# Kernel optimization log

Hardware: AMD Instinct MI355X
Metric: run time of the kernel (lower is better)

Reference implementation:

```python
import jax, jax.numpy as jnp
import numpy as np
from jax import lax

BN_EPS = 1e-5
SQ_EPS = 1e-8


def squash(s, axis=-1):
    # v = (|s|^2 / (1+|s|^2)) * s / |s|
    n2 = jnp.sum(s * s, axis=axis, keepdims=True)
    return (n2 / (1.0 + n2)) * s / jnp.sqrt(n2 + SQ_EPS)


def setup_inputs() -> dict:
    key = jax.random.key(0)
    ks = jax.random.split(key, 5)
    B, C, H, W = 64, 512, 28, 28
    NUM_ROUTES = 8 * 10 * 10  # lower_num_caps * 10 * 10 after k9 s2 conv on 28x28
    features = jax.random.normal(ks[0], (B, C, H, W), jnp.float32)
    conv1_w = jax.random.normal(ks[1], (256, 512, 3, 3), jnp.float32) * 0.02
    conv1_b = jnp.zeros((256,), jnp.float32)
    bn_gamma = jnp.ones((256,), jnp.float32)
    bn_beta = jnp.zeros((256,), jnp.float32)
    bn_mean = jnp.zeros((256,), jnp.float32)
    bn_var = jnp.ones((256,), jnp.float32)
    prim_w = jax.random.normal(ks[2], (256, 256, 9, 9), jnp.float32) * 0.02
    prim_b = jnp.zeros((256,), jnp.float32)
    # routing transform: (num_routes, higher_num_caps, out_dim, in_dim)
    route_w = jax.random.normal(ks[3], (NUM_ROUTES, 2, 16, 32), jnp.float32) * 0.05
    return {"features": features, "conv1_w": conv1_w, "conv1_b": conv1_b,
            "bn_gamma": bn_gamma, "bn_beta": bn_beta, "bn_mean": bn_mean,
            "bn_var": bn_var, "prim_w": prim_w, "prim_b": prim_b,
            "route_w": route_w}


def reference(features, conv1_w, conv1_b, bn_gamma, bn_beta, bn_mean, bn_var,
              prim_w, prim_b, route_w):
    B = features.shape[0]
    dn = ("NCHW", "OIHW", "NCHW")
    # pre_conv: Conv2d(512->256, k3, pad1) + BatchNorm (eval) + ReLU
    x = lax.conv_general_dilated(features, conv1_w, (1, 1), "SAME",
                                 dimension_numbers=dn)
    x = x + conv1_b[None, :, None, None]
    inv = bn_gamma * lax.rsqrt(bn_var + BN_EPS)
    x = x * inv[None, :, None, None] + (bn_beta - bn_mean * inv)[None, :, None, None]
    x = jax.nn.relu(x)
    # primary capsules: Conv2d(256->8*32, k9, s2, valid) -> (B,256,10,10)
    p = lax.conv_general_dilated(x, prim_w, (2, 2), "VALID",
                                 dimension_numbers=dn)
    p = p + prim_b[None, :, None, None]
    Hp, Wp = p.shape[2], p.shape[3]
    # (B, num_caps, cap_dim, Hp*Wp) -> (B, num_caps*Hp*Wp, cap_dim)
    p = p.reshape(B, 8, 32, Hp * Wp).transpose(0, 1, 3, 2).reshape(B, 8 * Hp * Wp, 32)
    lower_caps = squash(p, axis=-1)  # (B, 800, 32)
    # predictions u_hat: (B, routes, higher_caps, out_dim)
    u_hat = jnp.einsum("bri,rjoi->brjo", lower_caps, route_w)
    # dynamic routing-by-agreement
    b = jnp.zeros((B, u_hat.shape[1], u_hat.shape[2]), u_hat.dtype)
    n_iter = 3
    for it in range(n_iter):
        c = jax.nn.softmax(b, axis=2)                  # coupling coeffs
        s = jnp.einsum("brj,brjo->bjo", c, u_hat)      # weighted sum
        v = squash(s, axis=-1)                          # (B, 2, 16)
        if it < n_iter - 1:
            b = b + jnp.einsum("brjo,bjo->brj", u_hat, v)
    return (lower_caps, v)
```

## Files before the change

### kernel.cpp

```cpp
#include <hip/hip_runtime.h>
#include <hip/hip_bf16.h>

#define BN_EPS 1e-5f
#define SQ_EPS 1e-8f

typedef __hip_bfloat16 bf16;
typedef __attribute__((ext_vector_type(8))) short bf16x8;
typedef __attribute__((ext_vector_type(4))) float f32x4;

__device__ __forceinline__ void gload_lds16(const void* g, void* l) {
    __builtin_amdgcn_global_load_lds(
        (const __attribute__((address_space(1))) unsigned int*)g,
        (__attribute__((address_space(3))) unsigned int*)l, 16, 0, 0);
}

__device__ __forceinline__ unsigned short f2bfu(float f) {
    bf16 h = __float2bfloat16(f);
    return *(unsigned short*)&h;
}

__global__ __launch_bounds__(256) void feat_to_nhwc(
    const float* __restrict__ feat, bf16* __restrict__ featP) {
    int b = blockIdx.z, ct = blockIdx.y, pt = blockIdx.x;
    int ci0 = ct * 64, px0 = pt * 64;
    int tid = threadIdx.x;
    __shared__ float t[64][65];
#pragma unroll
    for (int rep = 0; rep < 16; rep++) {
        int ci_l = rep * 4 + (tid >> 6);
        int px = px0 + (tid & 63);
        float v = 0.f;
        if (px < 784) v = feat[(b * 512 + ci0 + ci_l) * 784 + px];
        t[ci_l][tid & 63] = v;
    }
    __syncthreads();
#pragma unroll
    for (int rep = 0; rep < 4; rep++) {
        int px_l = rep * 16 + (tid >> 4);
        int px = px0 + px_l;
        if (px < 784) {
            int h = px / 28, wq = px % 28;
            int ci = (tid & 15) * 4;
            ushort4 o;
            o.x = f2bfu(t[ci + 0][px_l]);
            o.y = f2bfu(t[ci + 1][px_l]);
            o.z = f2bfu(t[ci + 2][px_l]);
            o.w = f2bfu(t[ci + 3][px_l]);
            *(ushort4*)&featP[((b * 30 + h + 1) * 30 + (wq + 1)) * 512 + ci0 + ci] = o;
        }
    }
}

__global__ __launch_bounds__(128) void w1_transform(
    const float* __restrict__ w, bf16* __restrict__ wt1) {
    int co = blockIdx.y, ci0 = blockIdx.x * 32;
    __shared__ float t[288];
    const float* src = w + (co * 512 + ci0) * 9;
    for (int i = threadIdx.x; i < 288; i += 128) t[i] = src[i];
    __syncthreads();
    for (int i = threadIdx.x; i < 288; i += 128) {
        int kykx = i >> 5, ci = i & 31;
        wt1[(kykx * 256 + co) * 512 + ci0 + ci] = __float2bfloat16(t[ci * 9 + kykx]);
    }
}

__global__ __launch_bounds__(256) void w2_transform(
    const float* __restrict__ w, bf16* __restrict__ wt2) {
    int co = blockIdx.y, ci0 = blockIdx.x * 32;
    __shared__ float t[2592];
    const float* src = w + (co * 256 + ci0) * 81;
    for (int i = threadIdx.x; i < 2592; i += 256) t[i] = src[i];
    __syncthreads();
    for (int i = threadIdx.x; i < 2592; i += 256) {
        int kykx = i >> 5, ci = i & 31;
        wt2[(kykx * 256 + co) * 256 + ci0 + ci] = __float2bfloat16(t[ci * 81 + kykx]);
    }
}

__global__ __launch_bounds__(512, 2) void conv1_mfma(
    const bf16* __restrict__ featP, const bf16* __restrict__ wt1,
    const float* __restrict__ bias, const float* __restrict__ gamma,
    const float* __restrict__ beta, const float* __restrict__ mean,
    const float* __restrict__ var, bf16* __restrict__ x) {
    extern __shared__ char smem[];
    const int tid = threadIdx.x, lane = tid & 63, w = tid >> 6;
    const int wr = w >> 2, wc = w & 3;
    const int xcd = blockIdx.x & 7, ix = blockIdx.x >> 3;
    const int Mt = (xcd < 4 ? xcd * 25 : 100 + (xcd - 4) * 24) + ix;

    const bf16 *pA0, *pA1, *pB0, *pB1;
    {
        int r0 = (w << 4) + (lane >> 2);
        int q = (lane & 3) ^ ((r0 >> 1) & 3);
        int m0 = Mt * 256 + r0;
        int b0 = m0 / 784, rr = m0 % 784, h0 = rr / 28, w0 = rr % 28;
        pA0 = featP + ((b0 * 30 + h0) * 30 + w0) * 512 + q * 8;
        int m1 = m0 + 128;
        int b1 = m1 / 784, rr1 = m1 % 784, h1 = rr1 / 28, w1 = rr1 % 28;
        pA1 = featP + ((b1 * 30 + h1) * 30 + w1) * 512 + q * 8;
        pB0 = wt1 + r0 * 512 + q * 8;
        pB1 = pB0 + 128 * 512;
    }

    int a_off[8], b_off[4];
#pragma unroll
    for (int mi = 0; mi < 8; mi++) {
        int r = wr * 128 + mi * 16 + (lane & 15);
        a_off[mi] = r * 64 + (((lane >> 4) ^ ((r >> 1) & 3)) * 16);
    }
#pragma unroll
    for (int nj = 0; nj < 4; nj++) {
        int r = wc * 64 + nj * 16 + (lane & 15);
        b_off[nj] = r * 64 + (((lane >> 4) ^ ((r >> 1) & 3)) * 16);
    }

    f32x4 acc[8][4];
#pragma unroll
    for (int i = 0; i < 8; i++)
#pragma unroll
        for (int j = 0; j < 4; j++) acc[i][j] = f32x4{0.f, 0.f, 0.f, 0.f};

#define STG_A1(bi, oA)                                                      \
    do {                                                                    \
        gload_lds16(pA0 + (oA), smem + (bi) * 16384 + w * 1024);            \
        gload_lds16(pA1 + (oA), smem + (bi) * 16384 + 8192 + w * 1024);     \
    } while (0)
#define STG_B1(bi, oB)                                                      \
    do {                                                                    \
        gload_lds16(pB0 + (oB), smem + 65536 + (bi) * 16384 + w * 1024);    \
        gload_lds16(pB1 + (oB), smem + 65536 + (bi) * 16384 + 8192 + w * 1024); \
    } while (0)

    STG_A1(0, 0);  STG_B1(0, 0);
    STG_A1(1, 32); STG_B1(1, 32);
    STG_A1(2, 64); STG_B1(2, 64);
    asm volatile("s_waitcnt vmcnt(8)" ::: "memory");
    __builtin_amdgcn_s_barrier();
    asm volatile("" ::: "memory");

    for (int t = 0; t < 144; t += 4) {
#pragma unroll
        for (int u = 0; u < 4; u++) {
            const int cur = u, stg = (u + 3) & 3;
            const int tt = t + u + 3;
            const char* Ab = smem + cur * 16384;
            const char* Bb = smem + 65536 + cur * 16384;
            if (tt < 144) {
                int g = tt >> 4, cc = tt & 15;
                int ky = g / 3, kx = g - ky * 3;
                STG_A1(stg, (ky * 30 + kx) * 512 + cc * 32);
            }
            bf16x8 af[8];
#pragma unroll
            for (int mi = 0; mi < 8; mi++)
                af[mi] = *(const bf16x8*)(Ab + a_off[mi]);
            bf16x8 b0v = *(const bf16x8*)(Bb + b_off[0]);
            bf16x8 b1v = *(const bf16x8*)(Bb + b_off[1]);
            __builtin_amdgcn_s_setprio(1);
#pragma unroll
            for (int mi = 0; mi < 8; mi++)
                acc[mi][0] = __builtin_amdgcn_mfma_f32_16x16x32_bf16(af[mi], b0v, acc[mi][0], 0, 0, 0);
#pragma unroll
            for (int mi = 0; mi < 8; mi++)
                acc[mi][1] = __builtin_amdgcn_mfma_f32_16x16x32_bf16(af[mi], b1v, acc[mi][1], 0, 0, 0);
            __builtin_amdgcn_s_setprio(0);
            if (tt < 144) {
                int g = tt >> 4, cc = tt & 15;
                STG_B1(stg, g * 131072 + cc * 32);
            }
            bf16x8 b2v = *(const bf16x8*)(Bb + b_off[2]);
            bf16x8 b3v = *(const bf16x8*)(Bb + b_off[3]);
            __builtin_amdgcn_s_setprio(1);
#pragma unroll
            for (int mi = 0; mi < 8; mi++)
                acc[mi][2] = __builtin_amdgcn_mfma_f32_16x16x32_bf16(af[mi], b2v, acc[mi][2], 0, 0, 0);
#pragma unroll
            for (int mi = 0; mi < 8; mi++)
                acc[mi][3] = __builtin_amdgcn_mfma_f32_16x16x32_bf16(af[mi], b3v, acc[mi][3], 0, 0, 0);
            __builtin_amdgcn_s_setprio(0);
            if (tt < 144) asm volatile("s_waitcnt vmcnt(8)" ::: "memory");
            else          asm volatile("s_waitcnt vmcnt(0)" ::: "memory");
            __builtin_amdgcn_s_barrier();
            asm volatile("" ::: "memory");
        }
    }

#pragma unroll
    for (int nj = 0; nj < 4; nj++) {
        int co = wc * 64 + nj * 16 + (lane & 15);
        float inv = gamma[co] * rsqrtf(var[co] + BN_EPS);
        float sh = beta[co] - mean[co] * inv;
        float bs = bias[co];
#pragma unroll
        for (int mi = 0; mi < 8; mi++) {
            int m0 = Mt * 256 + wr * 128 + mi * 16 + ((lane >> 4) << 2);
#pragma unroll
            for (int r = 0; r < 4; r++) {
                float v = (acc[mi][nj][r] + bs) * inv + sh;
                x[(m0 + r) * 256 + co] = __float2bfloat16(fmaxf(v, 0.f));
            }
        }
    }
#undef STG_A1
#undef STG_B1
}

__global__ __launch_bounds__(512, 2) void conv2_mfma(
    const bf16* __restrict__ x, const bf16* __restrict__ wt2,
    bf16* __restrict__ p_parts) {
    extern __shared__ char smem[];
    const int tid = threadIdx.x, lane = tid & 63, w = tid >> 6;
    const int wr = w >> 2, wc = w & 3;
    const int z = blockIdx.x & 7, Mt = blockIdx.x >> 3;
    const int sh0 = (81 * z) >> 3, sh1 = (81 * (z + 1)) >> 3;
    const int NT = (sh1 - sh0) << 3;

    const bf16 *pA0, *pA1, *pB0, *pB1;
    {
        int r0 = (w << 4) + (lane >> 2);
        int q = (lane & 3) ^ ((r0 >> 1) & 3);
        int m0 = Mt * 256 + r0;
        int b0 = m0 / 100, s0 = m0 % 100, ho0 = s0 / 10, wo0 = s0 % 10;
        pA0 = x + ((b0 * 28 + 2 * ho0) * 28 + 2 * wo0) * 256 + q * 8;
        int m1 = m0 + 128;
        int b1 = m1 / 100, s1 = m1 % 100, ho1 = s1 / 10, wo1 = s1 % 10;
        pA1 = x + ((b1 * 28 + 2 * ho1) * 28 + 2 * wo1) * 256 + q * 8;
        pB0 = wt2 + r0 * 256 + q * 8;
        pB1 = pB0 + 128 * 256;
    }

    int a_off[8], b_off[4];
#pragma unroll
    for (int mi = 0; mi < 8; mi++) {
        int r = wr * 128 + mi * 16 + (lane & 15);
        a_off[mi] = r * 64 + (((lane >> 4) ^ ((r >> 1) & 3)) * 16);
    }
#pragma unroll
    for (int nj = 0; nj < 4; nj++) {
        int r = wc * 64 + nj * 16 + (lane & 15);
        b_off[nj] = r * 64 + (((lane >> 4) ^ ((r >> 1) & 3)) * 16);
    }

    f32x4 acc[8][4];
#pragma unroll
    for (int i = 0; i < 8; i++)
#pragma unroll
        for (int j = 0; j < 4; j++) acc[i][j] = f32x4{0.f, 0.f, 0.f, 0.f};

#define STG_A2(bi, oA)                                                      \
    do {                                                                    \
        gload_lds16(pA0 + (oA), smem + (bi) * 16384 + w * 1024);            \
        gload_lds16(pA1 + (oA), smem + (bi) * 16384 + 8192 + w * 1024);     \
    } while (0)
#define STG_B2(bi, oB)                                                      \
    do {                                                                    \
        gload_lds16(pB0 + (oB), smem + 65536 + (bi) * 16384 + w * 1024);    \
        gload_lds16(pB1 + (oB), smem + 65536 + (bi) * 16384 + 8192 + w * 1024); \
    } while (0)

    {
        int ky0 = sh0 / 9, kx0 = sh0 - 9 * ky0;
        int oA0 = (ky0 * 28 + kx0) * 256;
        int oB0 = sh0 * 65536;
        STG_A2(0, oA0);      STG_B2(0, oB0);
        STG_A2(1, oA0 + 32); STG_B2(1, oB0 + 32);
        STG_A2(2, oA0 + 64); STG_B2(2, oB0 + 64);
    }
    asm volatile("s_waitcnt vmcnt(8)" ::: "memory");
    __builtin_amdgcn_s_barrier();
    asm volatile("" ::: "memory");

    for (int t = 0; t < NT; t += 4) {
#pragma unroll
        for (int u = 0; u < 4; u++) {
            const int cur = u, stg = (u + 3) & 3;
            const int tt = t + u + 3;
            const char* Ab = smem + cur * 16384;
            const char* Bb = smem + 65536 + cur * 16384;
            if (tt < NT) {
                int sh = sh0 + (tt >> 3), cc = tt & 7;
                int ky = sh / 9, kx = sh - 9 * ky;
                STG_A2(stg, (ky * 28 + kx) * 256 + cc * 32);
            }
            bf16x8 af[8];
#pragma unroll
            for (int mi = 0; mi < 8; mi++)
                af[mi] = *(const bf16x8*)(Ab + a_off[mi]);
            bf16x8 b0v = *(const bf16x8*)(Bb + b_off[0]);
            bf16x8 b1v = *(const bf16x8*)(Bb + b_off[1]);
            __builtin_amdgcn_s_setprio(1);
#pragma unroll
            for (int mi = 0; mi < 8; mi++)
                acc[mi][0] = __builtin_amdgcn_mfma_f32_16x16x32_bf16(af[mi], b0v, acc[mi][0], 0, 0, 0);
#pragma unroll
            for (int mi = 0; mi < 8; mi++)
                acc[mi][1] = __builtin_amdgcn_mfma_f32_16x16x32_bf16(af[mi], b1v, acc[mi][1], 0, 0, 0);
            __builtin_amdgcn_s_setprio(0);
            if (tt < NT) {
                int sh = sh0 + (tt >> 3), cc = tt & 7;
                STG_B2(stg, sh * 65536 + cc * 32);
            }
            bf16x8 b2v = *(const bf16x8*)(Bb + b_off[2]);
            bf16x8 b3v = *(const bf16x8*)(Bb + b_off[3]);
            __builtin_amdgcn_s_setprio(1);
#pragma unroll
            for (int mi = 0; mi < 8; mi++)
                acc[mi][2] = __builtin_amdgcn_mfma_f32_16x16x32_bf16(af[mi], b2v, acc[mi][2], 0, 0, 0);
#pragma unroll
            for (int mi = 0; mi < 8; mi++)
                acc[mi][3] = __builtin_amdgcn_mfma_f32_16x16x32_bf16(af[mi], b3v, acc[mi][3], 0, 0, 0);
            __builtin_amdgcn_s_setprio(0);
            if (tt < NT) asm volatile("s_waitcnt vmcnt(8)" ::: "memory");
            else         asm volatile("s_waitcnt vmcnt(0)" ::: "memory");
            __builtin_amdgcn_s_barrier();
            asm volatile("" ::: "memory");
        }
    }

#pragma unroll
    for (int nj = 0; nj < 4; nj++) {
        int co = wc * 64 + nj * 16 + (lane & 15);
#pragma unroll
        for (int mi = 0; mi < 8; mi++) {
            int m0 = Mt * 256 + wr * 128 + mi * 16 + ((lane >> 4) << 2);
#pragma unroll
            for (int r = 0; r < 4; r++)
                p_parts[(z * 6400 + m0 + r) * 256 + co] =
                    __float2bfloat16(acc[mi][nj][r]);
        }
    }
#undef STG_A2
#undef STG_B2
}

__global__ __launch_bounds__(256) void squash_kernel(
    const bf16* __restrict__ pp, const float* __restrict__ pb,
    float* __restrict__ lc) {
    int rowg = blockIdx.x * 8 + (threadIdx.x >> 5);
    int i = threadIdx.x & 31;
    int b = rowg / 800, r = rowg - b * 800;
    int cap = r / 100, s = r - cap * 100;
    int m = b * 100 + s, co = cap * 32 + i;
    float val = pb[co];
#pragma unroll
    for (int z = 0; z < 8; z++)
        val += __bfloat162float(pp[(z * 6400 + m) * 256 + co]);
    float n2 = val * val;
#pragma unroll
    for (int msk = 1; msk < 32; msk <<= 1) n2 += __shfl_xor(n2, msk);
    float scale = n2 / ((1.f + n2) * sqrtf(n2 + SQ_EPS));
    lc[(b * 800 + r) * 32 + i] = val * scale;
}

__global__ __launch_bounds__(256) void uhat_kernel(
    const float* __restrict__ lc, const float* __restrict__ rw,
    float* __restrict__ uht) {
    int rT = blockIdx.x, bT = blockIdx.y;
    int rl = threadIdx.x >> 5, jo = threadIdx.x & 31;
    int r = rT * 8 + rl;
    float4 wreg[8];
    const float4* wp4 = reinterpret_cast<const float4*>(rw + (r * 32 + jo) * 32);
#pragma unroll
    for (int k = 0; k < 8; k++) wreg[k] = wp4[k];
    for (int b = bT * 16; b < bT * 16 + 16; b++) {
        const float4* lp4 = reinterpret_cast<const float4*>(lc + (b * 800 + r) * 32);
        float acc = 0.f;
#pragma unroll
        for (int k = 0; k < 8; k++) {
            float4 a = lp4[k];
            acc = fmaf(a.x, wreg[k].x, acc);
            acc = fmaf(a.y, wreg[k].y, acc);
            acc = fmaf(a.z, wreg[k].z, acc);
            acc = fmaf(a.w, wreg[k].w, acc);
        }
        uht[(b * 32 + jo) * 800 + r] = acc;
    }
}

__global__ __launch_bounds__(256) void route_sv_kernel(
    const float* __restrict__ uht, const float* __restrict__ bc,
    float* __restrict__ vbuf, float* __restrict__ vout,
    int first_iter, int write_out) {
    int b = blockIdx.y, j = blockIdx.x;
    int tid = threadIdx.x;
    float sp[16];
#pragma unroll
    for (int o = 0; o < 16; o++) sp[o] = 0.f;
    const float* u0 = uht + (b * 32 + j * 16) * 800;
    for (int r = tid; r < 800; r += 256) {
        float c;
        if (first_iter) {
            c = 0.5f;
        } else {
            float b0 = bc[(b * 800 + r) * 2 + 0];
            float b1 = bc[(b * 800 + r) * 2 + 1];
            float m = fmaxf(b0, b1);
            float e0 = __expf(b0 - m), e1 = __expf(b1 - m);
            c = (j == 0 ? e0 : e1) / (e0 + e1);
        }
#pragma unroll
        for (int o = 0; o < 16; o++) sp[o] += c * u0[o * 800 + r];
    }
#pragma unroll
    for (int o = 0; o < 16; o++)
#pragma unroll
        for (int m = 1; m < 64; m <<= 1) sp[o] += __shfl_xor(sp[o], m);
    __shared__ float red[4][16];
    int wave = tid >> 6;
    if ((tid & 63) == 0)
#pragma unroll
        for (int o = 0; o < 16; o++) red[wave][o] = sp[o];
    __syncthreads();
    if (tid == 0) {
        float s[16];
        float n2 = 0.f;
#pragma unroll
        for (int o = 0; o < 16; o++) {
            s[o] = red[0][o] + red[1][o] + red[2][o] + red[3][o];
            n2 += s[o] * s[o];
        }
        float scale = n2 / ((1.f + n2) * sqrtf(n2 + SQ_EPS));
#pragma unroll
        for (int o = 0; o < 16; o++) {
            float v = s[o] * scale;
            vbuf[(b * 2 + j) * 16 + o] = v;
            if (write_out) vout[(b * 2 + j) * 16 + o] = v;
        }
    }
}

__global__ __launch_bounds__(256) void route_bupd_kernel(
    const float* __restrict__ uht, const float* __restrict__ vbuf,
    float* __restrict__ bc) {
    int b = blockIdx.x;
    __shared__ float vs[32];
    if (threadIdx.x < 32) vs[threadIdx.x] = vbuf[b * 32 + threadIdx.x];
    __syncthreads();
    for (int r = threadIdx.x; r < 800; r += 256) {
#pragma unroll
        for (int j = 0; j < 2; j++) {
            float a = 0.f;
#pragma unroll
            for (int o = 0; o < 16; o++)
                a = fmaf(uht[(b * 32 + j * 16 + o) * 800 + r], vs[j * 16 + o], a);
            bc[(b * 800 + r) * 2 + j] += a;
        }
    }
}

extern "C" void kernel_launch(void* const* d_in, const int* in_sizes, int n_in,
                              void* d_out, int out_size, void* d_ws, size_t ws_size,
                              hipStream_t stream) {
    const float* feat    = (const float*)d_in[0];
    const float* conv1_w = (const float*)d_in[1];
    const float* conv1_b = (const float*)d_in[2];
    const float* bn_g    = (const float*)d_in[3];
    const float* bn_b    = (const float*)d_in[4];
    const float* bn_m    = (const float*)d_in[5];
    const float* bn_v    = (const float*)d_in[6];
    const float* prim_w  = (const float*)d_in[7];
    const float* prim_b  = (const float*)d_in[8];
    const float* route_w = (const float*)d_in[9];
    float* out = (float*)d_out;

    char* wsb = (char*)d_ws;
    bf16*  featP   = (bf16*)(wsb + 0);
    bf16*  p_parts = (bf16*)(wsb + 0);
    float* uht     = (float*)(wsb + 26214400);
    float* bc      = (float*)(wsb + 32768000);
    float* vbuf    = (float*)(wsb + 33177600);
    bf16*  x       = (bf16*)(wsb + 58982400);
    bf16*  wt1     = (bf16*)(wsb + 84672512);
    bf16*  wt2     = (bf16*)(wsb + 87031808);

    float* lc_out = out;
    float* v_out  = out + 64 * 800 * 32;

    hipFuncSetAttribute((const void*)conv1_mfma,
                        hipFuncAttributeMaxDynamicSharedMemorySize, 131072);
    hipFuncSetAttribute((const void*)conv2_mfma,
                        hipFuncAttributeMaxDynamicSharedMemorySize, 131072);

    hipMemsetAsync(featP, 0, 58982400, stream);
    feat_to_nhwc<<<dim3(13, 8, 64), 256, 0, stream>>>(feat, featP);
    w1_transform<<<dim3(16, 256), 128, 0, stream>>>(conv1_w, wt1);
    w2_transform<<<dim3(8, 256), 256, 0, stream>>>(prim_w, wt2);

    conv1_mfma<<<196, 512, 131072, stream>>>(
        featP, wt1, conv1_b, bn_g, bn_b, bn_m, bn_v, x);

    conv2_mfma<<<200, 512, 131072, stream>>>(x, wt2, p_parts);

    squash_kernel<<<64 * 800 / 8, 256, 0, stream>>>(p_parts, prim_b, lc_out);

    uhat_kernel<<<dim3(100, 4), 256, 0, stream>>>(lc_out, route_w, uht);

    hipMemsetAsync(bc, 0, 64 * 800 * 2 * sizeof(float), stream);

    route_sv_kernel<<<dim3(2, 64), 256, 0, stream>>>(uht, bc, vbuf, v_out, 1, 0);
    route_bupd_kernel<<<64, 256, 0, stream>>>(uht, vbuf, bc);
    route_sv_kernel<<<dim3(2, 64), 256, 0, stream>>>(uht, bc, vbuf, v_out, 0, 0);
    route_bupd_kernel<<<64, 256, 0, stream>>>(uht, vbuf, bc);
    route_sv_kernel<<<dim3(2, 64), 256, 0, stream>>>(uht, bc, vbuf, v_out, 0, 1);
}
```

Baseline: 311.8 us.

## Restructure convs to slab-reuse implicit GEMM and fuse routing into one kernel

Conv1 now stages one contiguous padded-pixel slab per channel chunk and reuses it across all 9 taps by offsetting LDS rows. Weights are pre-packed into MFMA fragment order and loaded straight from global into registers, with the next tile prefetched. Conv2 gets a similar slab staging over a channel-split x layout with per-batch M tiles. The full memset of the padded input is replaced by a kernel that zeroes only the border ring. The five routing launches are merged into one kernel per batch that keeps u_hat and the logits in LDS. The trade-off is wasted MFMA work on padded pixel rows and higher global weight-load traffic per wave.

```diff
diff --git a/kernel.cpp b/kernel.cpp
--- a/kernel.cpp
+++ b/kernel.cpp
@@ -51,286 +51,301 @@
     }
 }
 
-__global__ __launch_bounds__(128) void w1_transform(
-    const float* __restrict__ w, bf16* __restrict__ wt1) {
-    int co = blockIdx.y, ci0 = blockIdx.x * 32;
-    __shared__ float t[288];
-    const float* src = w + (co * 512 + ci0) * 9;
-    for (int i = threadIdx.x; i < 288; i += 128) t[i] = src[i];
+__global__ __launch_bounds__(256) void zero_ring(bf16* __restrict__ featP) {
+    int b = blockIdx.x;
+    uint4 zz = {0u, 0u, 0u, 0u};
+    for (int i = threadIdx.x; i < 116 * 64; i += 256) {
+        int rp = i >> 6;
+        int ci = (i & 63) * 8;
+        int hp, wp;
+        if (rp < 30)      { hp = 0;       wp = rp; }
+        else if (rp < 60) { hp = 29;      wp = rp - 30; }
+        else if (rp < 88) { hp = rp - 59; wp = 0; }
+        else              { hp = rp - 87; wp = 29; }
+        *(uint4*)&featP[(b * 900 + hp * 30 + wp) * 512 + ci] = zz;
+    }
+}
+
+__global__ __launch_bounds__(256) void w1F_transform(
+    const float* __restrict__ w, bf16* __restrict__ wt1F) {
+    int co = blockIdx.x;
+    __shared__ float t1[4608];
+    const float* src = w + co * 4608;
+    for (int i = threadIdx.x; i < 4608; i += 256) t1[i] = src[i];
     __syncthreads();
-    for (int i = threadIdx.x; i < 288; i += 128) {
-        int kykx = i >> 5, ci = i & 31;
-        wt1[(kykx * 256 + co) * 512 + ci0 + ci] = __float2bfloat16(t[ci * 9 + kykx]);
-    }
-}
-
-__global__ __launch_bounds__(256) void w2_transform(
-    const float* __restrict__ w, bf16* __restrict__ wt2) {
-    int co = blockIdx.y, ci0 = blockIdx.x * 32;
-    __shared__ float t[2592];
-    const float* src = w + (co * 256 + ci0) * 81;
-    for (int i = threadIdx.x; i < 2592; i += 256) t[i] = src[i];
+    int co16 = co >> 4, l15 = co & 15;
+    for (int i = threadIdx.x; i < 576; i += 256) {
+        int g = i >> 6, cc = (i >> 2) & 15, kq = i & 3;
+        short v[8];
+#pragma unroll
+        for (int j = 0; j < 8; j++) {
+            unsigned short u = f2bfu(t1[(cc * 32 + kq * 8 + j) * 9 + g]);
+            v[j] = (short)u;
+        }
+        int fidx = cc * 9 + g;
+        bf16x8* dst = (bf16x8*)&wt1F[(fidx * 16 + co16) * 512 + (kq * 16 + l15) * 8];
+        bf16x8 pk = {v[0], v[1], v[2], v[3], v[4], v[5], v[6], v[7]};
+        *dst = pk;
+    }
+}
+
+__global__ __launch_bounds__(256) void w2F_transform(
+    const float* __restrict__ w, bf16* __restrict__ wt2F) {
+    int half = blockIdx.x, co = blockIdx.y;
+    __shared__ float t2[10368];
+    const float* src = w + co * 20736 + half * 10368;
+    for (int i = threadIdx.x; i < 10368; i += 256) t2[i] = src[i];
     __syncthreads();
-    for (int i = threadIdx.x; i < 2592; i += 256) {
-        int kykx = i >> 5, ci = i & 31;
-        wt2[(kykx * 256 + co) * 256 + ci0 + ci] = __float2bfloat16(t[ci * 81 + kykx]);
+    int co16 = co >> 4, l15 = co & 15;
+    for (int i = threadIdx.x; i < 1296; i += 256) {
+        int sh = i >> 4, ccl = (i >> 2) & 3, kq = i & 3;
+        int z = sh / 10; if (z > 7) z = 7;
+        int s0 = (81 * z) >> 3;
+        int ns = ((81 * (z + 1)) >> 3) - s0;
+        int fidx = s0 * 8 + (half * 4 + ccl) * ns + (sh - s0);
+        short v[8];
+#pragma unroll
+        for (int j = 0; j < 8; j++) {
+            unsigned short u = f2bfu(t2[(ccl * 32 + kq * 8 + j) * 81 + sh]);
+            v[j] = (short)u;
+        }
+        bf16x8* dst = (bf16x8*)&wt2F[(fidx * 16 + co16) * 512 + (kq * 16 + l15) * 8];
+        bf16x8 pk = {v[0], v[1], v[2], v[3], v[4], v[5], v[6], v[7]};
+        *dst = pk;
     }
 }
 
 __global__ __launch_bounds__(512, 2) void conv1_mfma(
-    const bf16* __restrict__ featP, const bf16* __restrict__ wt1,
+    const bf16* __restrict__ featP, const bf16* __restrict__ wt1F,
     const float* __restrict__ bias, const float* __restrict__ gamma,
     const float* __restrict__ beta, const float* __restrict__ mean,
-    const float* __restrict__ var, bf16* __restrict__ x) {
-    extern __shared__ char smem[];
+    const float* __restrict__ var, bf16* __restrict__ x2) {
+    __shared__ short slab[2][10240];
     const int tid = threadIdx.x, lane = tid & 63, w = tid >> 6;
     const int wr = w >> 2, wc = w & 3;
-    const int xcd = blockIdx.x & 7, ix = blockIdx.x >> 3;
-    const int Mt = (xcd < 4 ? xcd * 25 : 100 + (xcd - 4) * 24) + ix;
-
-    const bf16 *pA0, *pA1, *pB0, *pB1;
+    const int Mt = blockIdx.x;
+    const int p0 = Mt * 256;
+
+    int srow = w * 16 + (lane >> 2);
+    int q = (lane & 3) ^ ((srow >> 1) & 3);
+    const bf16* pS = featP + (p0 + srow) * 512 + q * 8;
+
+    const bf16x8* pB = (const bf16x8*)wt1F + wc * 256 + lane;
+
+    int rm[8];
+#pragma unroll
+    for (int mi = 0; mi < 8; mi++) rm[mi] = wr * 128 + mi * 16 + (lane & 15);
+
+    f32x4 acc[8][4];
+#pragma unroll
+    for (int i = 0; i < 8; i++)
+#pragma unroll
+        for (int j = 0; j < 4; j++) acc[i][j] = f32x4{0.f, 0.f, 0.f, 0.f};
+
+#define STG1(bi, ccoff)                                                     \
+    do {                                                                    \
+        gload_lds16(pS + (ccoff), &slab[bi][w * 512]);                      \
+        gload_lds16(pS + (ccoff) + 65536, &slab[bi][w * 512 + 4096]);       \
+        if (w < 4)                                                          \
+            gload_lds16(pS + (ccoff) + 131072, &slab[bi][w * 512 + 8192]);  \
+    } while (0)
+
+    bf16x8 bcur[4], bnext[4];
+    STG1(0, 0);
     {
-        int r0 = (w << 4) + (lane >> 2);
-        int q = (lane & 3) ^ ((r0 >> 1) & 3);
-        int m0 = Mt * 256 + r0;
-        int b0 = m0 / 784, rr = m0 % 784, h0 = rr / 28, w0 = rr % 28;
-        pA0 = featP + ((b0 * 30 + h0) * 30 + w0) * 512 + q * 8;
-        int m1 = m0 + 128;
-        int b1 = m1 / 784, rr1 = m1 % 784, h1 = rr1 / 28, w1 = rr1 % 28;
-        pA1 = featP + ((b1 * 30 + h1) * 30 + w1) * 512 + q * 8;
-        pB0 = wt1 + r0 * 512 + q * 8;
-        pB1 = pB0 + 128 * 512;
-    }
-
-    int a_off[8], b_off[4];
-#pragma unroll
-    for (int mi = 0; mi < 8; mi++) {
-        int r = wr * 128 + mi * 16 + (lane & 15);
-        a_off[mi] = r * 64 + (((lane >> 4) ^ ((r >> 1) & 3)) * 16);
-    }
-#pragma unroll
-    for (int nj = 0; nj < 4; nj++) {
-        int r = wc * 64 + nj * 16 + (lane & 15);
-        b_off[nj] = r * 64 + (((lane >> 4) ^ ((r >> 1) & 3)) * 16);
-    }
-
-    f32x4 acc[8][4];
-#pragma unroll
-    for (int i = 0; i < 8; i++)
-#pragma unroll
-        for (int j = 0; j < 4; j++) acc[i][j] = f32x4{0.f, 0.f, 0.f, 0.f};
-
-#define STG_A1(bi, oA)                                                      \
-    do {                                                                    \
-        gload_lds16(pA0 + (oA), smem + (bi) * 16384 + w * 1024);            \
-        gload_lds16(pA1 + (oA), smem + (bi) * 16384 + 8192 + w * 1024);     \
-    } while (0)
-#define STG_B1(bi, oB)                                                      \
-    do {                                                                    \
-        gload_lds16(pB0 + (oB), smem + 65536 + (bi) * 16384 + w * 1024);    \
-        gload_lds16(pB1 + (oB), smem + 65536 + (bi) * 16384 + 8192 + w * 1024); \
-    } while (0)
-
-    STG_A1(0, 0);  STG_B1(0, 0);
-    STG_A1(1, 32); STG_B1(1, 32);
-    STG_A1(2, 64); STG_B1(2, 64);
-    asm volatile("s_waitcnt vmcnt(8)" ::: "memory");
+        const bf16x8* bp = pB;
+        bcur[0] = bp[0]; bcur[1] = bp[64]; bcur[2] = bp[128]; bcur[3] = bp[192];
+    }
+    asm volatile("s_waitcnt vmcnt(4)" ::: "memory");
     __builtin_amdgcn_s_barrier();
     asm volatile("" ::: "memory");
 
-    for (int t = 0; t < 144; t += 4) {
-#pragma unroll
-        for (int u = 0; u < 4; u++) {
-            const int cur = u, stg = (u + 3) & 3;
-            const int tt = t + u + 3;
-            const char* Ab = smem + cur * 16384;
-            const char* Bb = smem + 65536 + cur * 16384;
-            if (tt < 144) {
-                int g = tt >> 4, cc = tt & 15;
-                int ky = g / 3, kx = g - ky * 3;
-                STG_A1(stg, (ky * 30 + kx) * 512 + cc * 32);
+    for (int cc = 0; cc < 16; cc++) {
+        const char* sb = (const char*)slab[cc & 1];
+        const int OFFG[9] = {0, 1, 2, 30, 31, 32, 60, 61, 62};
+#pragma unroll
+        for (int g = 0; g < 9; g++) {
+            const int t = cc * 9 + g;
+            if (g == 0 && cc < 15) STG1((cc + 1) & 1, (cc + 1) * 32);
+            {
+                int tn = (t < 143) ? t + 1 : 143;
+                const bf16x8* bp = pB + tn * 1024;
+                bnext[0] = bp[0]; bnext[1] = bp[64];
+                bnext[2] = bp[128]; bnext[3] = bp[192];
             }
             bf16x8 af[8];
-#pragma unroll
-            for (int mi = 0; mi < 8; mi++)
-                af[mi] = *(const bf16x8*)(Ab + a_off[mi]);
-            bf16x8 b0v = *(const bf16x8*)(Bb + b_off[0]);
-            bf16x8 b1v = *(const bf16x8*)(Bb + b_off[1]);
+            const int og = OFFG[g];
+#pragma unroll
+            for (int mi = 0; mi < 8; mi++) {
+                int row = rm[mi] + og;
+                int ad = row * 64 + (((lane >> 4) ^ ((row >> 1) & 3)) << 4);
+                af[mi] = *(const bf16x8*)(sb + ad);
+            }
             __builtin_amdgcn_s_setprio(1);
 #pragma unroll
-            for (int mi = 0; mi < 8; mi++)
-                acc[mi][0] = __builtin_amdgcn_mfma_f32_16x16x32_bf16(af[mi], b0v, acc[mi][0], 0, 0, 0);
-#pragma unroll
-            for (int mi = 0; mi < 8; mi++)
-                acc[mi][1] = __builtin_amdgcn_mfma_f32_16x16x32_bf16(af[mi], b1v, acc[mi][1], 0, 0, 0);
+            for (int nj = 0; nj < 4; nj++)
+#pragma unroll
+                for (int mi = 0; mi < 8; mi++)
+                    acc[mi][nj] = __builtin_amdgcn_mfma_f32_16x16x32_bf16(
+                        af[mi], bcur[nj], acc[mi][nj], 0, 0, 0);
             __builtin_amdgcn_s_setprio(0);
-            if (tt < 144) {
-                int g = tt >> 4, cc = tt & 15;
-                STG_B1(stg, g * 131072 + cc * 32);
-            }
-            bf16x8 b2v = *(const bf16x8*)(Bb + b_off[2]);
-            bf16x8 b3v = *(const bf16x8*)(Bb + b_off[3]);
-            __builtin_amdgcn_s_setprio(1);
-#pragma unroll
-            for (int mi = 0; mi < 8; mi++)
-                acc[mi][2] = __builtin_amdgcn_mfma_f32_16x16x32_bf16(af[mi], b2v, acc[mi][2], 0, 0, 0);
-#pragma unroll
-            for (int mi = 0; mi < 8; mi++)
-                acc[mi][3] = __builtin_amdgcn_mfma_f32_16x16x32_bf16(af[mi], b3v, acc[mi][3], 0, 0, 0);
-            __builtin_amdgcn_s_setprio(0);
-            if (tt < 144) asm volatile("s_waitcnt vmcnt(8)" ::: "memory");
-            else          asm volatile("s_waitcnt vmcnt(0)" ::: "memory");
-            __builtin_amdgcn_s_barrier();
-            asm volatile("" ::: "memory");
-        }
-    }
-
+#pragma unroll
+            for (int i = 0; i < 4; i++) bcur[i] = bnext[i];
+        }
+        asm volatile("s_waitcnt vmcnt(4)" ::: "memory");
+        __builtin_amdgcn_s_barrier();
+        asm volatile("" ::: "memory");
+    }
+
+    float inv4[4], sh4[4], bs4[4];
+    int co4[4];
 #pragma unroll
     for (int nj = 0; nj < 4; nj++) {
         int co = wc * 64 + nj * 16 + (lane & 15);
-        float inv = gamma[co] * rsqrtf(var[co] + BN_EPS);
-        float sh = beta[co] - mean[co] * inv;
-        float bs = bias[co];
-#pragma unroll
-        for (int mi = 0; mi < 8; mi++) {
-            int m0 = Mt * 256 + wr * 128 + mi * 16 + ((lane >> 4) << 2);
+        co4[nj] = co;
+        inv4[nj] = gamma[co] * rsqrtf(var[co] + BN_EPS);
+        sh4[nj] = beta[co] - mean[co] * inv4[nj];
+        bs4[nj] = bias[co];
+    }
+    const int pbase = p0 + wr * 128 + ((lane >> 4) << 2);
+#pragma unroll
+    for (int mi = 0; mi < 8; mi++) {
+        int px[4]; bool val[4];
+#pragma unroll
+        for (int r = 0; r < 4; r++) {
+            int p = pbase + mi * 16 + r;
+            int bb = p / 900, rem = p - bb * 900;
+            int hh = rem / 30, ww = rem - hh * 30;
+            val[r] = (hh < 28) && (ww < 28);
+            px[r] = bb * 784 + hh * 28 + ww;
+        }
+#pragma unroll
+        for (int nj = 0; nj < 4; nj++) {
+            int co = co4[nj];
+            bf16* xb = x2 + (co >> 5) * 1605632 + (co & 31);
 #pragma unroll
             for (int r = 0; r < 4; r++) {
-                float v = (acc[mi][nj][r] + bs) * inv + sh;
-                x[(m0 + r) * 256 + co] = __float2bfloat16(fmaxf(v, 0.f));
-            }
-        }
-    }
-#undef STG_A1
-#undef STG_B1
+                if (val[r]) {
+                    float v = (acc[mi][nj][r] + bs4[nj]) * inv4[nj] + sh4[nj];
+                    xb[px[r] * 32] = __float2bfloat16(fmaxf(v, 0.f));
+                }
+            }
+        }
+    }
+#undef STG1
+}
+
+__device__ __forceinline__ void stage2(char* db, const bf16* pS, int ccoff, int w) {
+#pragma unroll
+    for (int k = 0; k < 9; k++) {
+        int L = w + 8 * k;
+        if (L < 70) {
+            int koff = k * 4096 + ((L >= 35) ? 7168 : 0);
+            gload_lds16(pS + ccoff + koff, db + k * 8192);
+        }
+    }
 }
 
 __global__ __launch_bounds__(512, 2) void conv2_mfma(
-    const bf16* __restrict__ x, const bf16* __restrict__ wt2,
+    const bf16* __restrict__ x2, const bf16* __restrict__ wt2F,
     bf16* __restrict__ p_parts) {
     extern __shared__ char smem[];
     const int tid = threadIdx.x, lane = tid & 63, w = tid >> 6;
     const int wr = w >> 2, wc = w & 3;
     const int z = blockIdx.x & 7, Mt = blockIdx.x >> 3;
-    const int sh0 = (81 * z) >> 3, sh1 = (81 * (z + 1)) >> 3;
-    const int NT = (sh1 - sh0) << 3;
-
-    const bf16 *pA0, *pA1, *pB0, *pB1;
+    const int sh0 = (81 * z) >> 3;
+    const int nsh = ((81 * (z + 1)) >> 3) - sh0;
+    const int ky0 = sh0 / 9;
+    const int b0 = Mt * 2;
+    const int pix00 = b0 * 784 + ky0 * 28;
+
+    int srow = w * 16 + (lane >> 2);
+    int q = (lane & 3) ^ ((srow >> 1) & 3);
+    const bf16* pS = x2 + (pix00 + srow) * 32 + q * 8;
+
+    const bf16x8* pB = (const bf16x8*)wt2F + wc * 256 + lane;
+
+    int basem[7];
+#pragma unroll
+    for (int mi = 0; mi < 7; mi++) {
+        int s = mi * 16 + (lane & 15);
+        int sc = s < 100 ? s : 99;
+        int ho = sc / 10, wo = sc - ho * 10;
+        basem[mi] = (wr * 20 + 2 * ho) * 28 + 2 * wo;
+    }
+
+    f32x4 acc[7][4];
+#pragma unroll
+    for (int i = 0; i < 7; i++)
+#pragma unroll
+        for (int j = 0; j < 4; j++) acc[i][j] = f32x4{0.f, 0.f, 0.f, 0.f};
+
+    bf16x8 bcur[4], bnext[4];
+    stage2(smem + w * 1024, pS, 0, w);
+    int f = sh0 * 8;
     {
-        int r0 = (w << 4) + (lane >> 2);
-        int q = (lane & 3) ^ ((r0 >> 1) & 3);
-        int m0 = Mt * 256 + r0;
-        int b0 = m0 / 100, s0 = m0 % 100, ho0 = s0 / 10, wo0 = s0 % 10;
-        pA0 = x + ((b0 * 28 + 2 * ho0) * 28 + 2 * wo0) * 256 + q * 8;
-        int m1 = m0 + 128;
-        int b1 = m1 / 100, s1 = m1 % 100, ho1 = s1 / 10, wo1 = s1 % 10;
-        pA1 = x + ((b1 * 28 + 2 * ho1) * 28 + 2 * wo1) * 256 + q * 8;
-        pB0 = wt2 + r0 * 256 + q * 8;
-        pB1 = pB0 + 128 * 256;
-    }
-
-    int a_off[8], b_off[4];
-#pragma unroll
-    for (int mi = 0; mi < 8; mi++) {
-        int r = wr * 128 + mi * 16 + (lane & 15);
-        a_off[mi] = r * 64 + (((lane >> 4) ^ ((r >> 1) & 3)) * 16);
-    }
-#pragma unroll
-    for (int nj = 0; nj < 4; nj++) {
-        int r = wc * 64 + nj * 16 + (lane & 15);
-        b_off[nj] = r * 64 + (((lane >> 4) ^ ((r >> 1) & 3)) * 16);
-    }
-
-    f32x4 acc[8][4];
-#pragma unroll
-    for (int i = 0; i < 8; i++)
-#pragma unroll
-        for (int j = 0; j < 4; j++) acc[i][j] = f32x4{0.f, 0.f, 0.f, 0.f};
-
-#define STG_A2(bi, oA)                                                      \
-    do {                                                                    \
-        gload_lds16(pA0 + (oA), smem + (bi) * 16384 + w * 1024);            \
-        gload_lds16(pA1 + (oA), smem + (bi) * 16384 + 8192 + w * 1024);     \
-    } while (0)
-#define STG_B2(bi, oB)                                                      \
-    do {                                                                    \
-        gload_lds16(pB0 + (oB), smem + 65536 + (bi) * 16384 + w * 1024);    \
-        gload_lds16(pB1 + (oB), smem + 65536 + (bi) * 16384 + 8192 + w * 1024); \
-    } while (0)
-
-    {
-        int ky0 = sh0 / 9, kx0 = sh0 - 9 * ky0;
-        int oA0 = (ky0 * 28 + kx0) * 256;
-        int oB0 = sh0 * 65536;
-        STG_A2(0, oA0);      STG_B2(0, oB0);
-        STG_A2(1, oA0 + 32); STG_B2(1, oB0 + 32);
-        STG_A2(2, oA0 + 64); STG_B2(2, oB0 + 64);
-    }
-    asm volatile("s_waitcnt vmcnt(8)" ::: "memory");
+        const bf16x8* bp = pB + f * 1024;
+        bcur[0] = bp[0]; bcur[1] = bp[64]; bcur[2] = bp[128]; bcur[3] = bp[192];
+    }
+    asm volatile("s_waitcnt vmcnt(4)" ::: "memory");
     __builtin_amdgcn_s_barrier();
     asm volatile("" ::: "memory");
 
-    for (int t = 0; t < NT; t += 4) {
-#pragma unroll
-        for (int u = 0; u < 4; u++) {
-            const int cur = u, stg = (u + 3) & 3;
-            const int tt = t + u + 3;
-            const char* Ab = smem + cur * 16384;
-            const char* Bb = smem + 65536 + cur * 16384;
-            if (tt < NT) {
-                int sh = sh0 + (tt >> 3), cc = tt & 7;
-                int ky = sh / 9, kx = sh - 9 * ky;
-                STG_A2(stg, (ky * 28 + kx) * 256 + cc * 32);
-            }
-            bf16x8 af[8];
-#pragma unroll
-            for (int mi = 0; mi < 8; mi++)
-                af[mi] = *(const bf16x8*)(Ab + a_off[mi]);
-            bf16x8 b0v = *(const bf16x8*)(Bb + b_off[0]);
-            bf16x8 b1v = *(const bf16x8*)(Bb + b_off[1]);
+    const int fmax = sh0 * 8 + 8 * nsh - 1;
+    for (int cc = 0; cc < 8; cc++) {
+        const char* sb = smem + (cc & 1) * 71680;
+        for (int si = 0; si < nsh; si++) {
+            if (si == 0 && cc < 7)
+                stage2(smem + ((cc + 1) & 1) * 71680 + w * 1024, pS,
+                       (cc + 1) * 1605632, w);
+            {
+                int fn = (f < fmax) ? f + 1 : fmax;
+                const bf16x8* bp = pB + fn * 1024;
+                bnext[0] = bp[0]; bnext[1] = bp[64];
+                bnext[2] = bp[128]; bnext[3] = bp[192];
+            }
+            int sh = sh0 + si;
+            int ky = sh / 9;
+            int og = (ky - ky0) * 28 + (sh - ky * 9);
+            bf16x8 af[7];
+#pragma unroll
+            for (int mi = 0; mi < 7; mi++) {
+                int row = basem[mi] + og;
+                int ad = row * 64 + (((lane >> 4) ^ ((row >> 1) & 3)) << 4);
+                af[mi] = *(const bf16x8*)(sb + ad);
+            }
             __builtin_amdgcn_s_setprio(1);
 #pragma unroll
-            for (int mi = 0; mi < 8; mi++)
-                acc[mi][0] = __builtin_amdgcn_mfma_f32_16x16x32_bf16(af[mi], b0v, acc[mi][0], 0, 0, 0);
-#pragma unroll
-            for (int mi = 0; mi < 8; mi++)
-                acc[mi][1] = __builtin_amdgcn_mfma_f32_16x16x32_bf16(af[mi], b1v, acc[mi][1], 0, 0, 0);
+            for (int nj = 0; nj < 4; nj++)
+#pragma unroll
+                for (int mi = 0; mi < 7; mi++)
+                    acc[mi][nj] = __builtin_amdgcn_mfma_f32_16x16x32_bf16(
+                        af[mi], bcur[nj], acc[mi][nj], 0, 0, 0);
             __builtin_amdgcn_s_setprio(0);
-            if (tt < NT) {
-                int sh = sh0 + (tt >> 3), cc = tt & 7;
-                STG_B2(stg, sh * 65536 + cc * 32);
-            }
-            bf16x8 b2v = *(const bf16x8*)(Bb + b_off[2]);
-            bf16x8 b3v = *(const bf16x8*)(Bb + b_off[3]);
-            __builtin_amdgcn_s_setprio(1);
-#pragma unroll
-            for (int mi = 0; mi < 8; mi++)
-                acc[mi][2] = __builtin_amdgcn_mfma_f32_16x16x32_bf16(af[mi], b2v, acc[mi][2], 0, 0, 0);
-#pragma unroll
-            for (int mi = 0; mi < 8; mi++)
-                acc[mi][3] = __builtin_amdgcn_mfma_f32_16x16x32_bf16(af[mi], b3v, acc[mi][3], 0, 0, 0);
-            __builtin_amdgcn_s_setprio(0);
-            if (tt < NT) asm volatile("s_waitcnt vmcnt(8)" ::: "memory");
-            else         asm volatile("s_waitcnt vmcnt(0)" ::: "memory");
-            __builtin_amdgcn_s_barrier();
-            asm volatile("" ::: "memory");
-        }
-    }
-
+#pragma unroll
+            for (int i = 0; i < 4; i++) bcur[i] = bnext[i];
+            f++;
+        }
+        asm volatile("s_waitcnt vmcnt(4)" ::: "memory");
+        __builtin_amdgcn_s_barrier();
+        asm volatile("" ::: "memory");
+    }
+
+    const int b = b0 + wr;
 #pragma unroll
     for (int nj = 0; nj < 4; nj++) {
         int co = wc * 64 + nj * 16 + (lane & 15);
 #pragma unroll
-        for (int mi = 0; mi < 8; mi++) {
-            int m0 = Mt * 256 + wr * 128 + mi * 16 + ((lane >> 4) << 2);
-#pragma unroll
-            for (int r = 0; r < 4; r++)
-                p_parts[(z * 6400 + m0 + r) * 256 + co] =
-                    __float2bfloat16(acc[mi][nj][r]);
-        }
-    }
-#undef STG_A2
-#undef STG_B2
+        for (int mi = 0; mi < 7; mi++) {
+#pragma unroll
+            for (int r = 0; r < 4; r++) {
+                int s = mi * 16 + ((lane >> 4) << 2) + r;
+                if (s < 100)
+                    p_parts[(z * 6400 + b * 100 + s) * 256 + co] =
+                        __float2bfloat16(acc[mi][nj][r]);
+            }
+        }
+    }
 }
 
 __global__ __launch_bounds__(256) void squash_kernel(
@@ -343,8 +358,8 @@
     int m = b * 100 + s, co = cap * 32 + i;
     float val = pb[co];
 #pragma unroll
-    for (int z = 0; z < 8; z++)
-        val += __bfloat162float(pp[(z * 6400 + m) * 256 + co]);
+    for (int zz = 0; zz < 8; zz++)
+        val += __bfloat162float(pp[(zz * 6400 + m) * 256 + co]);
     float n2 = val * val;
 #pragma unroll
     for (int msk = 1; msk < 32; msk <<= 1) n2 += __shfl_xor(n2, msk);
@@ -377,73 +392,57 @@
     }
 }
 
-__global__ __launch_bounds__(256) void route_sv_kernel(
-    const float* __restrict__ uht, const float* __restrict__ bc,
-    float* __restrict__ vbuf, float* __restrict__ vout,
-    int first_iter, int write_out) {
-    int b = blockIdx.y, j = blockIdx.x;
-    int tid = threadIdx.x;
-    float sp[16];
-#pragma unroll
-    for (int o = 0; o < 16; o++) sp[o] = 0.f;
-    const float* u0 = uht + (b * 32 + j * 16) * 800;
-    for (int r = tid; r < 800; r += 256) {
-        float c;
-        if (first_iter) {
-            c = 0.5f;
-        } else {
-            float b0 = bc[(b * 800 + r) * 2 + 0];
-            float b1 = bc[(b * 800 + r) * 2 + 1];
-            float m = fmaxf(b0, b1);
-            float e0 = __expf(b0 - m), e1 = __expf(b1 - m);
-            c = (j == 0 ? e0 : e1) / (e0 + e1);
-        }
-#pragma unroll
-        for (int o = 0; o < 16; o++) sp[o] += c * u0[o * 800 + r];
-    }
-#pragma unroll
-    for (int o = 0; o < 16; o++)
-#pragma unroll
-        for (int m = 1; m < 64; m <<= 1) sp[o] += __shfl_xor(sp[o], m);
-    __shared__ float red[4][16];
-    int wave = tid >> 6;
-    if ((tid & 63) == 0)
-#pragma unroll
-        for (int o = 0; o < 16; o++) red[wave][o] = sp[o];
+__global__ __launch_bounds__(256) void route_all(
+    const float* __restrict__ uht, float* __restrict__ vout) {
+    extern __shared__ float rs[];
+    float* u = rs;
+    float* lg = rs + 26400;
+    float* red = lg + 1600;
+    float* vs = red + 256;
+    int b = blockIdx.x, tid = threadIdx.x;
+    for (int i = tid; i < 25600; i += 256) {
+        int jo = i / 800, r = i - jo * 800;
+        u[r * 33 + jo] = uht[(b * 32 + jo) * 800 + r];
+    }
+    for (int i = tid; i < 1600; i += 256) lg[i] = 0.f;
     __syncthreads();
-    if (tid == 0) {
-        float s[16];
-        float n2 = 0.f;
-#pragma unroll
-        for (int o = 0; o < 16; o++) {
-            s[o] = red[0][o] + red[1][o] + red[2][o] + red[3][o];
-            n2 += s[o] * s[o];
-        }
-        float scale = n2 / ((1.f + n2) * sqrtf(n2 + SQ_EPS));
-#pragma unroll
-        for (int o = 0; o < 16; o++) {
-            float v = s[o] * scale;
-            vbuf[(b * 2 + j) * 16 + o] = v;
-            if (write_out) vout[(b * 2 + j) * 16 + o] = v;
-        }
-    }
-}
-
-__global__ __launch_bounds__(256) void route_bupd_kernel(
-    const float* __restrict__ uht, const float* __restrict__ vbuf,
-    float* __restrict__ bc) {
-    int b = blockIdx.x;
-    __shared__ float vs[32];
-    if (threadIdx.x < 32) vs[threadIdx.x] = vbuf[b * 32 + threadIdx.x];
-    __syncthreads();
-    for (int r = threadIdx.x; r < 800; r += 256) {
-#pragma unroll
-        for (int j = 0; j < 2; j++) {
-            float a = 0.f;
-#pragma unroll
-            for (int o = 0; o < 16; o++)
-                a = fmaf(uht[(b * 32 + j * 16 + o) * 800 + r], vs[j * 16 + o], a);
-            bc[(b * 800 + r) * 2 + j] += a;
+    int jo = tid & 31, rg = tid >> 5;
+    for (int it = 0; it < 3; it++) {
+        float sp = 0.f;
+        for (int r = rg; r < 800; r += 8) {
+            float l0 = lg[r * 2], l1 = lg[r * 2 + 1];
+            float m = fmaxf(l0, l1);
+            float e0 = __expf(l0 - m), e1 = __expf(l1 - m);
+            float c = ((jo < 16) ? e0 : e1) / (e0 + e1);
+            sp += c * u[r * 33 + jo];
+        }
+        red[rg * 32 + jo] = sp;
+        __syncthreads();
+        if (tid < 32) {
+            float s = 0.f;
+#pragma unroll
+            for (int k = 0; k < 8; k++) s += red[k * 32 + tid];
+            float n2 = s * s;
+#pragma unroll
+            for (int m = 1; m < 16; m <<= 1) n2 += __shfl_xor(n2, m);
+            float scale = n2 / ((1.f + n2) * sqrtf(n2 + SQ_EPS));
+            float v = s * scale;
+            vs[tid] = v;
+            if (it == 2) vout[b * 32 + tid] = v;
+        }
+        __syncthreads();
+        if (it < 2) {
+            for (int r = tid; r < 800; r += 256) {
+                float d0 = 0.f, d1 = 0.f;
+#pragma unroll
+                for (int o = 0; o < 16; o++) {
+                    d0 += u[r * 33 + o] * vs[o];
+                    d1 += u[r * 33 + 16 + o] * vs[16 + o];
+                }
+                lg[r * 2] += d0;
+                lg[r * 2 + 1] += d1;
+            }
+            __syncthreads();
         }
     }
 }
@@ -467,39 +466,31 @@
     bf16*  featP   = (bf16*)(wsb + 0);
     bf16*  p_parts = (bf16*)(wsb + 0);
     float* uht     = (float*)(wsb + 26214400);
-    float* bc      = (float*)(wsb + 32768000);
-    float* vbuf    = (float*)(wsb + 33177600);
-    bf16*  x       = (bf16*)(wsb + 58982400);
-    bf16*  wt1     = (bf16*)(wsb + 84672512);
-    bf16*  wt2     = (bf16*)(wsb + 87031808);
+    bf16*  x2      = (bf16*)(wsb + 58982400);
+    bf16*  wt1F    = (bf16*)(wsb + 84672512);
+    bf16*  wt2F    = (bf16*)(wsb + 87031808);
 
     float* lc_out = out;
     float* v_out  = out + 64 * 800 * 32;
 
-    hipFuncSetAttribute((const void*)conv1_mfma,
-                        hipFuncAttributeMaxDynamicSharedMemorySize, 131072);
     hipFuncSetAttribute((const void*)conv2_mfma,
-                        hipFuncAttributeMaxDynamicSharedMemorySize, 131072);
-
-    hipMemsetAsync(featP, 0, 58982400, stream);
+                        hipFuncAttributeMaxDynamicSharedMemorySize, 143360);
+    hipFuncSetAttribute((const void*)route_all,
+                        hipFuncAttributeMaxDynamicSharedMemorySize, 113152);
+
     feat_to_nhwc<<<dim3(13, 8, 64), 256, 0, stream>>>(feat, featP);
-    w1_transform<<<dim3(16, 256), 128, 0, stream>>>(conv1_w, wt1);
-    w2_transform<<<dim3(8, 256), 256, 0, stream>>>(prim_w, wt2);
-
-    conv1_mfma<<<196, 512, 131072, stream>>>(
-        featP, wt1, conv1_b, bn_g, bn_b, bn_m, bn_v, x);
-
-    conv2_mfma<<<200, 512, 131072, stream>>>(x, wt2, p_parts);
-
-    squash_kernel<<<64 * 800 / 8, 256, 0, stream>>>(p_parts, prim_b, lc_out);
+    zero_ring<<<64, 256, 0, stream>>>(featP);
+    w1F_transform<<<256, 256, 0, stream>>>(conv1_w, wt1F);
+    w2F_transform<<<dim3(2, 256), 256, 0, stream>>>(prim_w, wt2F);
+
+    conv1_mfma<<<225, 512, 0, stream>>>(
+        featP, wt1F, conv1_b, bn_g, bn_b, bn_m, bn_v, x2);
+
+    conv2_mfma<<<256, 512, 143360, stream>>>(x2, wt2F, p_parts);
+
+    squash_kernel<<<6400, 256, 0, stream>>>(p_parts, prim_b, lc_out);
 
     uhat_kernel<<<dim3(100, 4), 256, 0, stream>>>(lc_out, route_w, uht);
 
-    hipMemsetAsync(bc, 0, 64 * 800 * 2 * sizeof(float), stream);
-
-    route_sv_kernel<<<dim3(2, 64), 256, 0, stream>>>(uht, bc, vbuf, v_out, 1, 0);
-    route_bupd_kernel<<<64, 256, 0, stream>>>(uht, vbuf, bc);
-    route_sv_kernel<<<dim3(2, 64), 256, 0, stream>>>(uht, bc, vbuf, v_out, 0, 0);
-    route_bupd_kernel<<<64, 256, 0, stream>>>(uht, vbuf, bc);
-    route_sv_kernel<<<dim3(2, 64), 256, 0, stream>>>(uht, bc, vbuf, v_out, 0, 1);
-}
+    route_all<<<64, 256, 113152, stream>>>(uht, v_out);
+}
```

Measured after the change: 410.0 us. 1.31x slower.
